# Kernel tuning notes

Hardware: AMD Instinct MI355X
Metric: run time of the kernel (lower is better)

The kernel has to match this reference:

```python
import jax, jax.numpy as jnp
import numpy as np

N = 100000
E = 3200000
K = 10
ALPHA = 0.1
EPS = 1e-5


def setup_inputs() -> dict:
    key = jax.random.key(0)
    ks = jax.random.split(key, 12)
    x = jax.random.normal(ks[0], (N, 512), dtype=jnp.float32)
    edge_index = jax.random.randint(ks[1], (2, E), 0, N, dtype=jnp.int32)
    w1 = jax.random.normal(ks[2], (128, 512), dtype=jnp.float32) * 0.02
    b1 = jnp.zeros((128,), jnp.float32)
    g1 = jnp.ones((128,), jnp.float32)
    be1 = jnp.zeros((128,), jnp.float32)
    m1 = jax.random.normal(ks[3], (128,), dtype=jnp.float32) * 0.1
    v1 = jax.random.uniform(ks[4], (128,), dtype=jnp.float32, minval=0.5, maxval=1.5)
    w2 = jax.random.normal(ks[5], (128, 128), dtype=jnp.float32) * 0.02
    b2 = jnp.zeros((128,), jnp.float32)
    g2 = jnp.ones((128,), jnp.float32)
    be2 = jnp.zeros((128,), jnp.float32)
    m2 = jax.random.normal(ks[6], (128,), dtype=jnp.float32) * 0.1
    v2 = jax.random.uniform(ks[7], (128,), dtype=jnp.float32, minval=0.5, maxval=1.5)
    w3 = jax.random.normal(ks[8], (3, 128), dtype=jnp.float32) * 0.02
    b3 = jnp.zeros((3,), jnp.float32)
    return dict(x=x, edge_index=edge_index, w1=w1, b1=b1, g1=g1, be1=be1, m1=m1, v1=v1,
                w2=w2, b2=b2, g2=g2, be2=be2, m2=m2, v2=v2, w3=w3, b3=b3)


def _bn(y, g, be, m, v):
    return (y - m) * jax.lax.rsqrt(v + EPS) * g + be


def reference(x, edge_index, w1, b1, g1, be1, m1, v1, w2, b2, g2, be2, m2, v2, w3, b3):
    # MLP (eval mode: BN uses running stats, dropout is identity)
    h = jax.nn.relu(_bn(x @ w1.T + b1, g1, be1, m1, v1))
    h = h + jax.nn.relu(_bn(h @ w2.T + b2, g2, be2, m2, v2))
    h = h @ w3.T + b3  # [N, 3]

    # APPNP propagation with GCN normalization + self-loops
    loop = jnp.arange(N, dtype=edge_index.dtype)
    src = jnp.concatenate([edge_index[0], loop])
    dst = jnp.concatenate([edge_index[1], loop])
    deg = jax.ops.segment_sum(jnp.ones_like(src, dtype=h.dtype), dst, num_segments=N)
    dinv = jnp.where(deg > 0, jax.lax.rsqrt(deg), 0.0)
    norm = dinv[src] * dinv[dst]  # [E+N]

    h0 = h
    z = h
    for _ in range(K):
        msg = z[src] * norm[:, None]
        z = jax.ops.segment_sum(msg, dst, num_segments=N)
        z = (1.0 - ALPHA) * z + ALPHA * h0
    return jax.nn.log_softmax(z, axis=1)
```

## Files before the change

### kernel.cpp

```cpp
#include <hip/hip_runtime.h>
#include <cstdint>
#include <cstddef>

#define N_NODES 100000
#define D_IN 512
#define ALPHA 0.1f
#define EPS_BN 1e-5f
#define M_TILE 128
#define BK 64

#define CBITS 8
#define CNODES 256
#define NCBIN 391
#define TILE 8192
#define EPT 32
#define BINCAP 9216

#define NPB 64
#define NB2 1563
#define LCAP3 3072

typedef float f32x4 __attribute__((ext_vector_type(4)));
typedef __bf16 bf16x8 __attribute__((ext_vector_type(8)));
typedef unsigned short u16x8 __attribute__((ext_vector_type(8)));
typedef unsigned short u16x4 __attribute__((ext_vector_type(4)));

__device__ __forceinline__ unsigned short f2bf(float f) {
  unsigned u = __float_as_uint(f);
  u += 0x7fffu + ((u >> 16) & 1u);
  return (unsigned short)(u >> 16);
}
__device__ __forceinline__ float bf2f(unsigned short h) {
  return __uint_as_float(((unsigned)h) << 16);
}

__global__ void k_prep(const float* __restrict__ w1, const float* __restrict__ b1,
                       const float* __restrict__ g1, const float* __restrict__ be1,
                       const float* __restrict__ m1, const float* __restrict__ v1,
                       const float* __restrict__ w2, const float* __restrict__ b2,
                       const float* __restrict__ g2, const float* __restrict__ be2,
                       const float* __restrict__ m2, const float* __restrict__ v2,
                       unsigned short* __restrict__ w1b, unsigned short* __restrict__ w2b,
                       float* __restrict__ bias1, float* __restrict__ bias2,
                       int* __restrict__ bincur) {
  int idx = blockIdx.x * 256 + threadIdx.x;
  if (idx < 65536) {
    int n = idx >> 9;
    float s = g1[n] * rsqrtf(v1[n] + EPS_BN);
    w1b[idx] = f2bf(w1[idx] * s);
  } else if (idx < 81920) {
    int i = idx - 65536;
    int n = i >> 7;
    float s = g2[n] * rsqrtf(v2[n] + EPS_BN);
    w2b[i] = f2bf(w2[i] * s);
  } else if (idx < 82048) {
    int c = idx - 81920;
    float s = g1[c] * rsqrtf(v1[c] + EPS_BN);
    bias1[c] = (b1[c] - m1[c]) * s + be1[c];
  } else if (idx < 82176) {
    int c = idx - 82048;
    float s = g2[c] * rsqrtf(v2[c] + EPS_BN);
    bias2[c] = (b2[c] - m2[c]) * s + be2[c];
  }
  int bi = idx - 82176;
  if (bi >= 0 && bi < NCBIN) bincur[bi] = 0;
}

#define NB_SCAN 391
__global__ void k_scan2(const int* __restrict__ bincur, int* __restrict__ bsum) {
  __shared__ int s[448];
  int t = threadIdx.x;
  for (int i = t; i < 448; i += 256) s[i] = (i < NB_SCAN) ? bincur[i] : 0;
  __syncthreads();
  if (t < 64) {
    int base = t * 7;
    int vals[7];
    int sum = 0;
#pragma unroll
    for (int j = 0; j < 7; ++j) { vals[j] = s[base + j]; sum += vals[j]; }
    int x = sum;
#pragma unroll
    for (int off = 1; off < 64; off <<= 1) {
      int y = __shfl_up(x, off, 64);
      if (t >= off) x += y;
    }
    int run = x - sum;
#pragma unroll
    for (int j = 0; j < 7; ++j) { int tmp = vals[j]; s[base + j] = run; run += tmp; }
  }
  __syncthreads();
  for (int i = t; i < NB_SCAN; i += 256) bsum[i] = s[i];
}

__global__ void k_scan3(const int* __restrict__ deg, const int* __restrict__ bsum,
                        int* __restrict__ row_start, float* __restrict__ dinv, int E) {
  __shared__ int sb[2][256];
  int t = threadIdx.x;
  int i = blockIdx.x * 256 + t;
  int d = (i < N_NODES) ? deg[i] : 0;
  sb[0][t] = d;
  __syncthreads();
  int cur = 0;
#pragma unroll
  for (int off = 1; off < 256; off <<= 1) {
    int val = sb[cur][t] + ((t >= off) ? sb[cur][t - off] : 0);
    sb[cur ^ 1][t] = val;
    __syncthreads();
    cur ^= 1;
  }
  int incl = sb[cur][t];
  int ex = incl - d;
  if (i < N_NODES) {
    int rs = bsum[blockIdx.x] + ex;
    row_start[i] = rs;
    dinv[i] = rsqrtf((float)(d + 1));
  }
  if (i == N_NODES) row_start[N_NODES] = E;
}

__global__ __launch_bounds__(256) void k_binA(const int* __restrict__ src,
                                              const int* __restrict__ dst, int E,
                                              int* __restrict__ bincur,
                                              unsigned* __restrict__ binned) {
  __shared__ unsigned stage[TILE];
  __shared__ int cnt[NCBIN];
  __shared__ int loff[NCBIN + 1];
  __shared__ int goff[NCBIN];
  __shared__ int sc[2][256];
  const int tid = threadIdx.x;

  for (int i = tid; i < NCBIN; i += 256) cnt[i] = 0;
  __syncthreads();

  const int e0 = blockIdx.x * TILE;
  const int n = min(TILE, E - e0);

  unsigned pk[EPT];
  int bp[EPT];
#pragma unroll
  for (int i = 0; i < EPT; ++i) {
    int o = i * 256 + tid;
    if (o < n) {
      int e = e0 + o;
      int d = dst[e];
      int s = src[e];
      int b = d >> CBITS;
      pk[i] = (unsigned)s | ((unsigned)(d & (CNODES - 1)) << 17);
      int p = atomicAdd(&cnt[b], 1);
      bp[i] = b | (p << 9);
    } else bp[i] = -1;
  }
  __syncthreads();

  int c0 = (2 * tid     < NCBIN) ? cnt[2 * tid]     : 0;
  int c1 = (2 * tid + 1 < NCBIN) ? cnt[2 * tid + 1] : 0;
  sc[0][tid] = c0 + c1;
  __syncthreads();
  int cur = 0;
#pragma unroll
  for (int off = 1; off < 256; off <<= 1) {
    sc[cur ^ 1][tid] = sc[cur][tid] + ((tid >= off) ? sc[cur][tid - off] : 0);
    __syncthreads();
    cur ^= 1;
  }
  int ex = sc[cur][tid] - (c0 + c1);
  if (2 * tid < NCBIN) loff[2 * tid] = ex;
  if (2 * tid + 1 < NCBIN) loff[2 * tid + 1] = ex + c0;
  if (tid == 255) loff[NCBIN] = sc[cur][255];
  __syncthreads();
  for (int i = tid; i < NCBIN; i += 256)
    if (cnt[i] > 0) goff[i] = atomicAdd(&bincur[i], cnt[i]);
  __syncthreads();

#pragma unroll
  for (int i = 0; i < EPT; ++i) {
    if (bp[i] >= 0) {
      int b = bp[i] & 511;
      int p = bp[i] >> 9;
      stage[loff[b] + p] = pk[i];
    }
  }
  __syncthreads();

  for (int i = tid; i < n; i += 256) {
    int lo = 0, hi = NCBIN;
    while (hi - lo > 1) { int mid = (lo + hi) >> 1; if (loff[mid] <= i) lo = mid; else hi = mid; }
    int b = lo;
    binned[(size_t)b * BINCAP + goff[b] + (i - loff[b])] = stage[i];
  }
}

__global__ __launch_bounds__(256) void k_binB1(const unsigned* __restrict__ binned,
                                               const int* __restrict__ bincur,
                                               int* __restrict__ deg) {
  __shared__ int lcnt[CNODES];
  int b = blockIdx.x;
  int t = threadIdx.x;
  lcnt[t] = 0;
  __syncthreads();
  int cnt = bincur[b];
  const unsigned* bp = binned + (size_t)b * BINCAP;
  for (int i = t; i < cnt; i += 256) {
    unsigned v = bp[i];
    atomicAdd(&lcnt[v >> 17], 1);
  }
  __syncthreads();
  int node = (b << CBITS) + t;
  if (node < N_NODES) deg[node] = lcnt[t];
}

__global__ __launch_bounds__(256) void k_binB2(const unsigned* __restrict__ binned,
                                               const int* __restrict__ bincur,
                                               const int* __restrict__ row_start,
                                               unsigned* __restrict__ csr_col) {
  __shared__ unsigned sortbuf[BINCAP];
  __shared__ int lcur[CNODES];
  int b = blockIdx.x;
  int t = threadIdx.x;
  int node0 = b << CBITS;
  int nodes = min(CNODES, N_NODES - node0);
  int rs0 = row_start[node0];
  if (t < nodes) lcur[t] = row_start[node0 + t] - rs0;
  __syncthreads();
  int cnt = bincur[b];
  const unsigned* bp = binned + (size_t)b * BINCAP;
  for (int i = t; i < cnt; i += 256) {
    unsigned v = bp[i];
    int p = atomicAdd(&lcur[v >> 17], 1);
    sortbuf[p] = v & 0x1FFFFu;
  }
  __syncthreads();
  for (int i = t; i < cnt; i += 256) csr_col[rs0 + i] = sortbuf[i];
}

__global__ __launch_bounds__(256, 2) void k_mlp(
    const float* __restrict__ x, const unsigned short* __restrict__ w1b,
    const unsigned short* __restrict__ w2b, const float* __restrict__ bias1,
    const float* __restrict__ bias2, const float* __restrict__ w3,
    const float* __restrict__ b3, const float* __restrict__ dinv,
    float4* __restrict__ h0, float4* __restrict__ zt) {
  __shared__ unsigned short arena[35840];
  __shared__ float lds_w3[384];
  unsigned short* lds_x = arena;
  unsigned short* lds_w = arena + 9216;
  unsigned short* lds_h = arena;
  unsigned short* lds_w2 = arena + 18432;

  const int tid = threadIdx.x;
  const int lane = tid & 63;
  const int wv = tid >> 6;
  const int fr = lane & 15;
  const int kq = (lane >> 4) * 8;
  const int rq = (lane >> 4) * 4;
  const int row0 = blockIdx.x * M_TILE;

  for (int i = tid; i < 384; i += 256) lds_w3[i] = w3[i];

#pragma unroll
  for (int it = 0; it < 8; ++it) {
    int idx = it * 256 + tid;
    int n = idx >> 4, c8 = idx & 15;
    uint4 v = *(const uint4*)(w2b + n * 128 + c8 * 8);
    *(uint4*)(lds_w2 + n * 136 + c8 * 8) = v;
  }

  const int xr_r = 0, xr_c = 0; (void)xr_r; (void)xr_c;
  f32x4 xr[8];
#pragma unroll
  for (int it = 0; it < 8; ++it) {
    int idx = it * 256 + tid;
    int r = idx >> 4, c4 = idx & 15;
    int gm = row0 + r;
    if (gm >= N_NODES) gm = N_NODES - 1;
    xr[it] = *(const f32x4*)(x + (size_t)gm * D_IN + 0 + c4 * 4);
  }

  f32x4 zero4 = {0.f, 0.f, 0.f, 0.f};
  f32x4 acc[2][8];
#pragma unroll
  for (int mt = 0; mt < 2; ++mt)
#pragma unroll
    for (int nt = 0; nt < 8; ++nt) acc[mt][nt] = zero4;

  for (int kb = 0; kb < D_IN; kb += BK) {
#pragma unroll
    for (int it = 0; it < 8; ++it) {
      int idx = it * 256 + tid;
      int r = idx >> 4, c4 = idx & 15;
      u16x4 o;
      o.x = f2bf(xr[it].x); o.y = f2bf(xr[it].y); o.z = f2bf(xr[it].z); o.w = f2bf(xr[it].w);
      *(u16x4*)(lds_x + r * 72 + c4 * 4) = o;
    }
#pragma unroll
    for (int it = 0; it < 4; ++it) {
      int idx = it * 256 + tid;
      int n = idx >> 3, c8 = idx & 7;
      uint4 v = *(const uint4*)(w1b + n * 512 + kb + c8 * 8);
      *(uint4*)(lds_w + n * 72 + c8 * 8) = v;
    }
    __syncthreads();
    if (kb + BK < D_IN) {
#pragma unroll
      for (int it = 0; it < 8; ++it) {
        int idx = it * 256 + tid;
        int r = idx >> 4, c4 = idx & 15;
        int gm = row0 + r;
        if (gm >= N_NODES) gm = N_NODES - 1;
        xr[it] = *(const f32x4*)(x + (size_t)gm * D_IN + (kb + BK) + c4 * 4);
      }
    }
#pragma unroll
    for (int kk = 0; kk < BK; kk += 32) {
      bf16x8 a[2], b[8];
#pragma unroll
      for (int mt = 0; mt < 2; ++mt)
        a[mt] = __builtin_bit_cast(bf16x8, *(const u16x8*)(lds_x + (wv * 32 + mt * 16 + fr) * 72 + kk + kq));
#pragma unroll
      for (int nt = 0; nt < 8; ++nt)
        b[nt] = __builtin_bit_cast(bf16x8, *(const u16x8*)(lds_w + (nt * 16 + fr) * 72 + kk + kq));
#pragma unroll
      for (int mt = 0; mt < 2; ++mt)
#pragma unroll
        for (int nt = 0; nt < 8; ++nt)
          acc[mt][nt] = __builtin_amdgcn_mfma_f32_16x16x32_bf16(a[mt], b[nt], acc[mt][nt], 0, 0, 0);
    }
    __syncthreads();
  }

  float b1v[8], b2v[8];
#pragma unroll
  for (int nt = 0; nt < 8; ++nt) {
    b1v[nt] = bias1[nt * 16 + fr];
    b2v[nt] = bias2[nt * 16 + fr];
  }
  float hr[2][8][4];
#pragma unroll
  for (int mt = 0; mt < 2; ++mt)
#pragma unroll
    for (int nt = 0; nt < 8; ++nt)
#pragma unroll
      for (int r = 0; r < 4; ++r) {
        int rl = wv * 32 + mt * 16 + rq + r;
        int cl = nt * 16 + fr;
        float h = acc[mt][nt][r] + b1v[nt];
        h = h > 0.f ? h : 0.f;
        hr[mt][nt][r] = h;
        lds_h[rl * 136 + cl] = f2bf(h);
      }
  __syncthreads();

  f32x4 acc2[2][8];
#pragma unroll
  for (int mt = 0; mt < 2; ++mt)
#pragma unroll
    for (int nt = 0; nt < 8; ++nt) acc2[mt][nt] = zero4;
#pragma unroll
  for (int kk = 0; kk < 128; kk += 32) {
    bf16x8 a[2], b[8];
#pragma unroll
    for (int mt = 0; mt < 2; ++mt)
      a[mt] = __builtin_bit_cast(bf16x8, *(const u16x8*)(lds_h + (wv * 32 + mt * 16 + fr) * 136 + kk + kq));
#pragma unroll
    for (int nt = 0; nt < 8; ++nt)
      b[nt] = __builtin_bit_cast(bf16x8, *(const u16x8*)(lds_w2 + (nt * 16 + fr) * 136 + kk + kq));
#pragma unroll
    for (int mt = 0; mt < 2; ++mt)
#pragma unroll
      for (int nt = 0; nt < 8; ++nt)
        acc2[mt][nt] = __builtin_amdgcn_mfma_f32_16x16x32_bf16(a[mt], b[nt], acc2[mt][nt], 0, 0, 0);
  }
  __syncthreads();

#pragma unroll
  for (int mt = 0; mt < 2; ++mt)
#pragma unroll
    for (int nt = 0; nt < 8; ++nt)
#pragma unroll
      for (int r = 0; r < 4; ++r) {
        int rl = wv * 32 + mt * 16 + rq + r;
        int cl = nt * 16 + fr;
        float t2 = acc2[mt][nt][r] + b2v[nt];
        t2 = t2 > 0.f ? t2 : 0.f;
        lds_h[rl * 136 + cl] = f2bf(hr[mt][nt][r] + t2);
      }
  __syncthreads();

  if (tid < 128) {
    int m = tid;
    int gm = row0 + m;
    if (gm < N_NODES) {
      float a0 = 0.f, a1 = 0.f, a2 = 0.f;
#pragma unroll 8
      for (int c = 0; c < 128; ++c) {
        float hv = bf2f(lds_h[m * 136 + c]);
        a0 += hv * lds_w3[c];
        a1 += hv * lds_w3[128 + c];
        a2 += hv * lds_w3[256 + c];
      }
      float z0 = a0 + b3[0], z1 = a1 + b3[1], z2 = a2 + b3[2];
      float di = dinv[gm];
      h0[gm] = make_float4(z0, z1, z2, 0.f);
      zt[gm] = make_float4(di * z0, di * z1, di * z2, 0.f);
    }
  }
}

#define GATHER_BODY(IDX)                                                        \
  for (; j + 8 <= je; j += 8) {                                                 \
    unsigned c0 = IDX(j + 0), c1 = IDX(j + 1), c2 = IDX(j + 2), c3 = IDX(j + 3);\
    unsigned c4 = IDX(j + 4), c5 = IDX(j + 5), c6 = IDX(j + 6), c7 = IDX(j + 7);\
    float4 v0 = zin[c0], v1 = zin[c1], v2 = zin[c2], v3 = zin[c3];              \
    float4 v4 = zin[c4], v5 = zin[c5], v6 = zin[c6], v7 = zin[c7];              \
    sx += ((v0.x + v1.x) + (v2.x + v3.x)) + ((v4.x + v5.x) + (v6.x + v7.x));    \
    sy += ((v0.y + v1.y) + (v2.y + v3.y)) + ((v4.y + v5.y) + (v6.y + v7.y));    \
    sz += ((v0.z + v1.z) + (v2.z + v3.z)) + ((v4.z + v5.z) + (v6.z + v7.z));    \
  }                                                                             \
  if (j + 4 <= je) {                                                            \
    unsigned c0 = IDX(j + 0), c1 = IDX(j + 1), c2 = IDX(j + 2), c3 = IDX(j + 3);\
    float4 v0 = zin[c0], v1 = zin[c1], v2 = zin[c2], v3 = zin[c3];              \
    sx += (v0.x + v1.x) + (v2.x + v3.x);                                        \
    sy += (v0.y + v1.y) + (v2.y + v3.y);                                        \
    sz += (v0.z + v1.z) + (v2.z + v3.z);                                        \
    j += 4;                                                                     \
  }                                                                             \
  if (j + 2 <= je) {                                                            \
    unsigned c0 = IDX(j + 0), c1 = IDX(j + 1);                                  \
    float4 v0 = zin[c0], v1 = zin[c1];                                          \
    sx += v0.x + v1.x; sy += v0.y + v1.y; sz += v0.z + v1.z;                    \
    j += 2;                                                                     \
  }                                                                             \
  if (j < je) {                                                                 \
    float4 v = zin[IDX(j)];                                                     \
    sx += v.x; sy += v.y; sz += v.z;                                            \
  }

template <bool FINAL>
__global__ __launch_bounds__(256) void k_iter2(
    const float4* __restrict__ zin, float4* __restrict__ zout,
    const int* __restrict__ row_start, const unsigned* __restrict__ csr_col,
    const float* __restrict__ dinv, const float4* __restrict__ h0v,
    float* __restrict__ out) {
  __shared__ unsigned lidx[LCAP3];
  __shared__ float psum[3][NPB][3];
  __shared__ int srs[2];
  const int t = threadIdx.x;
  const int q = t >> 6;
  const int tn = t & 63;
  const int node0 = blockIdx.x * NPB;
  const int node = node0 + tn;
  const bool valid = node < N_NODES;

  if (t == 0) srs[0] = row_start[node0];
  if (t == 1) srs[1] = row_start[min(node0 + NPB, N_NODES)];
  __syncthreads();
  const int rs0 = srs[0];
  const int cnt = srs[1] - rs0;
  const bool use_lds = (cnt <= LCAP3);
  if (use_lds) {
    for (int i = t; i < cnt; i += 256) lidx[i] = csr_col[rs0 + i];
  }

  int jb = 0, je = 0;
  if (valid) {
    int r0 = row_start[node];
    int r1 = row_start[node + 1];
    int len = r1 - r0;
    jb = r0 + ((len * q) >> 2);
    je = r0 + ((len * (q + 1)) >> 2);
  }
  __syncthreads();

  float sx = 0.f, sy = 0.f, sz = 0.f;
  if (use_lds) {
    int j = jb - rs0;
    je -= rs0;
#define IDXL(J) lidx[J]
    GATHER_BODY(IDXL)
#undef IDXL
  } else {
    int j = jb;
#define IDXG(J) csr_col[J]
    GATHER_BODY(IDXG)
#undef IDXG
  }

  if (q) { psum[q - 1][tn][0] = sx; psum[q - 1][tn][1] = sy; psum[q - 1][tn][2] = sz; }
  __syncthreads();
  if (q == 0 && valid) {
    float4 self = zin[node];
    float4 h = h0v[node];
    float di = dinv[node];
    sx += (psum[0][tn][0] + psum[1][tn][0]) + (psum[2][tn][0] + self.x);
    sy += (psum[0][tn][1] + psum[1][tn][1]) + (psum[2][tn][1] + self.y);
    sz += (psum[0][tn][2] + psum[1][tn][2]) + (psum[2][tn][2] + self.z);
    float zx = (1.f - ALPHA) * di * sx + ALPHA * h.x;
    float zy = (1.f - ALPHA) * di * sy + ALPHA * h.y;
    float zz = (1.f - ALPHA) * di * sz + ALPHA * h.z;
    if (!FINAL) {
      zout[node] = make_float4(di * zx, di * zy, di * zz, 0.f);
    } else {
      float mx = fmaxf(zx, fmaxf(zy, zz));
      float l = logf(expf(zx - mx) + expf(zy - mx) + expf(zz - mx));
      out[node * 3 + 0] = zx - mx - l;
      out[node * 3 + 1] = zy - mx - l;
      out[node * 3 + 2] = zz - mx - l;
    }
  }
}

extern "C" void kernel_launch(void* const* d_in, const int* in_sizes, int n_in,
                              void* d_out, int out_size, void* d_ws, size_t ws_size,
                              hipStream_t stream) {
  const float* x   = (const float*)d_in[0];
  const int*   ei  = (const int*)d_in[1];
  const float* w1  = (const float*)d_in[2];
  const float* b1  = (const float*)d_in[3];
  const float* g1  = (const float*)d_in[4];
  const float* be1 = (const float*)d_in[5];
  const float* m1  = (const float*)d_in[6];
  const float* v1  = (const float*)d_in[7];
  const float* w2  = (const float*)d_in[8];
  const float* b2  = (const float*)d_in[9];
  const float* g2  = (const float*)d_in[10];
  const float* be2 = (const float*)d_in[11];
  const float* m2  = (const float*)d_in[12];
  const float* v2  = (const float*)d_in[13];
  const float* w3  = (const float*)d_in[14];
  const float* b3  = (const float*)d_in[15];

  const int E = in_sizes[1] / 2;
  const int* srcA = ei;
  const int* dstA = ei + E;

  char* w = (char*)d_ws;
  size_t off = 0;
  auto alloc = [&](size_t bytes) -> void* {
    void* p = w + off;
    off = (off + bytes + 255) & ~(size_t)255;
    return p;
  };
  unsigned short* w1b   = (unsigned short*)alloc(65536 * 2);
  unsigned short* w2b   = (unsigned short*)alloc(16384 * 2);
  float* bias1          = (float*)alloc(128 * 4);
  float* bias2          = (float*)alloc(128 * 4);
  int*   deg            = (int*)alloc((size_t)N_NODES * 4);
  int*   row_start      = (int*)alloc(((size_t)N_NODES + 1) * 4);
  float* dinv           = (float*)alloc((size_t)N_NODES * 4);
  int*   bsum           = (int*)alloc(512 * 4);
  int*   bincur         = (int*)alloc((size_t)NCBIN * 4);
  float4* h0            = (float4*)alloc((size_t)N_NODES * 16);
  float4* ztA           = (float4*)alloc((size_t)N_NODES * 16);
  float4* ztB           = (float4*)alloc((size_t)N_NODES * 16);
  unsigned* csr_col     = (unsigned*)alloc((size_t)E * 4);
  unsigned* binned      = (unsigned*)alloc((size_t)NCBIN * BINCAP * 4);

  const int NB = (N_NODES + 255) / 256;
  const int NTILE = (E + TILE - 1) / TILE;

  k_prep<<<(82176 + NCBIN + 255) / 256, 256, 0, stream>>>(
      w1, b1, g1, be1, m1, v1, w2, b2, g2, be2, m2, v2, w1b, w2b, bias1, bias2, bincur);
  k_binA<<<NTILE, 256, 0, stream>>>(srcA, dstA, E, bincur, binned);
  k_binB1<<<NCBIN, 256, 0, stream>>>(binned, bincur, deg);
  k_scan2<<<1, 256, 0, stream>>>(bincur, bsum);
  k_scan3<<<NB, 256, 0, stream>>>(deg, bsum, row_start, dinv, E);
  k_binB2<<<NCBIN, 256, 0, stream>>>(binned, bincur, row_start, csr_col);
  k_mlp<<<(N_NODES + M_TILE - 1) / M_TILE, 256, 0, stream>>>(
      x, w1b, w2b, bias1, bias2, w3, b3, dinv, h0, ztA);

  const float4* zin = ztA;
  float4* zout = ztB;
  for (int k = 0; k < 9; ++k) {
    k_iter2<false><<<NB2, 256, 0, stream>>>(zin, zout, row_start, csr_col, dinv, h0, nullptr);
    const float4* tswap = zout;
    zout = (float4*)zin;
    zin = tswap;
  }
  k_iter2<true><<<NB2, 256, 0, stream>>>(zin, nullptr, row_start, csr_col, dinv, h0, (float*)d_out);
}
```

Before: 596.5 us.

## Balance APPNP gather by splitting each block's edge range evenly across threads

Replaces the per-node, four-way split gather with an edge-balanced scheme. Each thread takes a contiguous slice of the block's edges staged in LDS, issues up to 12 independent loads up front, and binary-searches the row offsets to find its starting node. Partial sums are then flushed into per-node LDS accumulators with shared-memory atomics. This aims to remove load imbalance between nodes and raise memory-level parallelism, at the cost of redundant clamped loads, LDS atomic contention and a summation order that is no longer fixed.

```diff
diff --git a/kernel.cpp b/kernel.cpp
--- a/kernel.cpp
+++ b/kernel.cpp
@@ -19,6 +19,7 @@
 #define NPB 64
 #define NB2 1563
 #define LCAP3 3072
+#define PMAX 12
 
 typedef float f32x4 __attribute__((ext_vector_type(4)));
 typedef __bf16 bf16x8 __attribute__((ext_vector_type(8)));
@@ -264,7 +265,6 @@
     *(uint4*)(lds_w2 + n * 136 + c8 * 8) = v;
   }
 
-  const int xr_r = 0, xr_c = 0; (void)xr_r; (void)xr_c;
   f32x4 xr[8];
 #pragma unroll
   for (int it = 0; it < 8; ++it) {
@@ -405,94 +405,87 @@
   }
 }
 
-#define GATHER_BODY(IDX)                                                        \
-  for (; j + 8 <= je; j += 8) {                                                 \
-    unsigned c0 = IDX(j + 0), c1 = IDX(j + 1), c2 = IDX(j + 2), c3 = IDX(j + 3);\
-    unsigned c4 = IDX(j + 4), c5 = IDX(j + 5), c6 = IDX(j + 6), c7 = IDX(j + 7);\
-    float4 v0 = zin[c0], v1 = zin[c1], v2 = zin[c2], v3 = zin[c3];              \
-    float4 v4 = zin[c4], v5 = zin[c5], v6 = zin[c6], v7 = zin[c7];              \
-    sx += ((v0.x + v1.x) + (v2.x + v3.x)) + ((v4.x + v5.x) + (v6.x + v7.x));    \
-    sy += ((v0.y + v1.y) + (v2.y + v3.y)) + ((v4.y + v5.y) + (v6.y + v7.y));    \
-    sz += ((v0.z + v1.z) + (v2.z + v3.z)) + ((v4.z + v5.z) + (v6.z + v7.z));    \
-  }                                                                             \
-  if (j + 4 <= je) {                                                            \
-    unsigned c0 = IDX(j + 0), c1 = IDX(j + 1), c2 = IDX(j + 2), c3 = IDX(j + 3);\
-    float4 v0 = zin[c0], v1 = zin[c1], v2 = zin[c2], v3 = zin[c3];              \
-    sx += (v0.x + v1.x) + (v2.x + v3.x);                                        \
-    sy += (v0.y + v1.y) + (v2.y + v3.y);                                        \
-    sz += (v0.z + v1.z) + (v2.z + v3.z);                                        \
-    j += 4;                                                                     \
-  }                                                                             \
-  if (j + 2 <= je) {                                                            \
-    unsigned c0 = IDX(j + 0), c1 = IDX(j + 1);                                  \
-    float4 v0 = zin[c0], v1 = zin[c1];                                          \
-    sx += v0.x + v1.x; sy += v0.y + v1.y; sz += v0.z + v1.z;                    \
-    j += 2;                                                                     \
-  }                                                                             \
-  if (j < je) {                                                                 \
-    float4 v = zin[IDX(j)];                                                     \
-    sx += v.x; sy += v.y; sz += v.z;                                            \
-  }
-
 template <bool FINAL>
-__global__ __launch_bounds__(256) void k_iter2(
+__global__ __launch_bounds__(256) void k_iter3(
     const float4* __restrict__ zin, float4* __restrict__ zout,
     const int* __restrict__ row_start, const unsigned* __restrict__ csr_col,
     const float* __restrict__ dinv, const float4* __restrict__ h0v,
     float* __restrict__ out) {
   __shared__ unsigned lidx[LCAP3];
-  __shared__ float psum[3][NPB][3];
-  __shared__ int srs[2];
+  __shared__ int row_off[NPB + 1];
+  __shared__ float accs[NPB][3];
   const int t = threadIdx.x;
-  const int q = t >> 6;
-  const int tn = t & 63;
   const int node0 = blockIdx.x * NPB;
-  const int node = node0 + tn;
-  const bool valid = node < N_NODES;
-
-  if (t == 0) srs[0] = row_start[node0];
-  if (t == 1) srs[1] = row_start[min(node0 + NPB, N_NODES)];
-  __syncthreads();
-  const int rs0 = srs[0];
-  const int cnt = srs[1] - rs0;
-  const bool use_lds = (cnt <= LCAP3);
-  if (use_lds) {
+  const int node = node0 + t;
+
+  if (t <= NPB) row_off[t] = row_start[min(node0 + t, N_NODES)];
+  if (t < NPB) { accs[t][0] = 0.f; accs[t][1] = 0.f; accs[t][2] = 0.f; }
+  __syncthreads();
+  const int rs0 = row_off[0];
+  const int cnt = row_off[NPB] - rs0;
+
+  if (cnt <= LCAP3) {
     for (int i = t; i < cnt; i += 256) lidx[i] = csr_col[rs0 + i];
-  }
-
-  int jb = 0, je = 0;
-  if (valid) {
-    int r0 = row_start[node];
-    int r1 = row_start[node + 1];
-    int len = r1 - r0;
-    jb = r0 + ((len * q) >> 2);
-    je = r0 + ((len * (q + 1)) >> 2);
-  }
-  __syncthreads();
-
-  float sx = 0.f, sy = 0.f, sz = 0.f;
-  if (use_lds) {
-    int j = jb - rs0;
-    je -= rs0;
-#define IDXL(J) lidx[J]
-    GATHER_BODY(IDXL)
-#undef IDXL
+    __syncthreads();
+
+    const int per = (cnt + 255) >> 8;
+    const int e0 = t * per;
+    const int e1 = min(e0 + per, cnt);
+    if (e0 < e1) {
+      f32x4 v[PMAX];
+#pragma unroll
+      for (int i = 0; i < PMAX; ++i) {
+        int e = e0 + i;
+        unsigned c = lidx[(e < e1) ? e : (e1 - 1)];
+        v[i] = *(const f32x4*)(zin + c);
+      }
+      int lo = 0, hi = NPB;
+      while (hi - lo > 1) {
+        int m = (lo + hi) >> 1;
+        if (row_off[m] - rs0 <= e0) lo = m; else hi = m;
+      }
+      int r = lo;
+      int nb = row_off[r + 1] - rs0;
+      float sx = 0.f, sy = 0.f, sz = 0.f;
+#pragma unroll
+      for (int i = 0; i < PMAX; ++i) {
+        int e = e0 + i;
+        if (e < e1) {
+          while (e >= nb) {
+            atomicAdd(&accs[r][0], sx);
+            atomicAdd(&accs[r][1], sy);
+            atomicAdd(&accs[r][2], sz);
+            sx = 0.f; sy = 0.f; sz = 0.f;
+            ++r;
+            nb = row_off[r + 1] - rs0;
+          }
+          sx += v[i].x; sy += v[i].y; sz += v[i].z;
+        }
+      }
+      atomicAdd(&accs[r][0], sx);
+      atomicAdd(&accs[r][1], sy);
+      atomicAdd(&accs[r][2], sz);
+    }
   } else {
-    int j = jb;
-#define IDXG(J) csr_col[J]
-    GATHER_BODY(IDXG)
-#undef IDXG
-  }
-
-  if (q) { psum[q - 1][tn][0] = sx; psum[q - 1][tn][1] = sy; psum[q - 1][tn][2] = sz; }
-  __syncthreads();
-  if (q == 0 && valid) {
+    if (t < NPB && node < N_NODES) {
+      int r0 = row_start[node], r1 = row_start[node + 1];
+      float sx = 0.f, sy = 0.f, sz = 0.f;
+      for (int j = r0; j < r1; ++j) {
+        float4 vv = zin[csr_col[j]];
+        sx += vv.x; sy += vv.y; sz += vv.z;
+      }
+      accs[t][0] = sx; accs[t][1] = sy; accs[t][2] = sz;
+    }
+  }
+  __syncthreads();
+
+  if (t < NPB && node < N_NODES) {
     float4 self = zin[node];
     float4 h = h0v[node];
     float di = dinv[node];
-    sx += (psum[0][tn][0] + psum[1][tn][0]) + (psum[2][tn][0] + self.x);
-    sy += (psum[0][tn][1] + psum[1][tn][1]) + (psum[2][tn][1] + self.y);
-    sz += (psum[0][tn][2] + psum[1][tn][2]) + (psum[2][tn][2] + self.z);
+    float sx = accs[t][0] + self.x;
+    float sy = accs[t][1] + self.y;
+    float sz = accs[t][2] + self.z;
     float zx = (1.f - ALPHA) * di * sx + ALPHA * h.x;
     float zy = (1.f - ALPHA) * di * sy + ALPHA * h.y;
     float zz = (1.f - ALPHA) * di * sz + ALPHA * h.z;
@@ -570,10 +563,10 @@
   const float4* zin = ztA;
   float4* zout = ztB;
   for (int k = 0; k < 9; ++k) {
-    k_iter2<false><<<NB2, 256, 0, stream>>>(zin, zout, row_start, csr_col, dinv, h0, nullptr);
+    k_iter3<false><<<NB2, 256, 0, stream>>>(zin, zout, row_start, csr_col, dinv, h0, nullptr);
     const float4* tswap = zout;
     zout = (float4*)zin;
     zin = tswap;
   }
-  k_iter2<true><<<NB2, 256, 0, stream>>>(zin, nullptr, row_start, csr_col, dinv, h0, (float*)d_out);
-}
+  k_iter3<true><<<NB2, 256, 0, stream>>>(zin, nullptr, row_start, csr_col, dinv, h0, (float*)d_out);
+}
```

After: 668.0 us. 1.12x slower.

## Store propagated features as packed fp16 and fuse CSR build kernels

Applied to the files above, without the earlier changes.

The propagation state z is now stored as three fp16 values packed into 8 bytes instead of a float4. This halves the bytes moved by each random gather in the ten propagation iterations. Separately, the degree count, the two scan kernels and the CSR scatter are merged into one per-bin kernel, which computes its prefix offset by summing earlier bin counts directly. Using fp16 adds rounding error to the iterated values, and each block now does a redundant partial sum over bincur.

```diff
diff --git a/kernel.cpp b/kernel.cpp
--- a/kernel.cpp
+++ b/kernel.cpp
@@ -24,6 +24,7 @@
 typedef __bf16 bf16x8 __attribute__((ext_vector_type(8)));
 typedef unsigned short u16x8 __attribute__((ext_vector_type(8)));
 typedef unsigned short u16x4 __attribute__((ext_vector_type(4)));
+typedef unsigned long long u64;
 
 __device__ __forceinline__ unsigned short f2bf(float f) {
   unsigned u = __float_as_uint(f);
@@ -32,6 +33,19 @@
 }
 __device__ __forceinline__ float bf2f(unsigned short h) {
   return __uint_as_float(((unsigned)h) << 16);
+}
+
+__device__ __forceinline__ u64 pk3(float x, float y, float z) {
+  unsigned short a = __builtin_bit_cast(unsigned short, (_Float16)x);
+  unsigned short b = __builtin_bit_cast(unsigned short, (_Float16)y);
+  unsigned short c = __builtin_bit_cast(unsigned short, (_Float16)z);
+  return (u64)a | ((u64)b << 16) | ((u64)c << 32);
+}
+__device__ __forceinline__ void up3(u64 p, float& sx, float& sy, float& sz) {
+  unsigned lo = (unsigned)p, hi = (unsigned)(p >> 32);
+  sx += (float)__builtin_bit_cast(_Float16, (unsigned short)(lo & 0xFFFFu));
+  sy += (float)__builtin_bit_cast(_Float16, (unsigned short)(lo >> 16));
+  sz += (float)__builtin_bit_cast(_Float16, (unsigned short)(hi & 0xFFFFu));
 }
 
 __global__ void k_prep(const float* __restrict__ w1, const float* __restrict__ b1,
@@ -66,58 +80,6 @@
   if (bi >= 0 && bi < NCBIN) bincur[bi] = 0;
 }
 
-#define NB_SCAN 391
-__global__ void k_scan2(const int* __restrict__ bincur, int* __restrict__ bsum) {
-  __shared__ int s[448];
-  int t = threadIdx.x;
-  for (int i = t; i < 448; i += 256) s[i] = (i < NB_SCAN) ? bincur[i] : 0;
-  __syncthreads();
-  if (t < 64) {
-    int base = t * 7;
-    int vals[7];
-    int sum = 0;
-#pragma unroll
-    for (int j = 0; j < 7; ++j) { vals[j] = s[base + j]; sum += vals[j]; }
-    int x = sum;
-#pragma unroll
-    for (int off = 1; off < 64; off <<= 1) {
-      int y = __shfl_up(x, off, 64);
-      if (t >= off) x += y;
-    }
-    int run = x - sum;
-#pragma unroll
-    for (int j = 0; j < 7; ++j) { int tmp = vals[j]; s[base + j] = run; run += tmp; }
-  }
-  __syncthreads();
-  for (int i = t; i < NB_SCAN; i += 256) bsum[i] = s[i];
-}
-
-__global__ void k_scan3(const int* __restrict__ deg, const int* __restrict__ bsum,
-                        int* __restrict__ row_start, float* __restrict__ dinv, int E) {
-  __shared__ int sb[2][256];
-  int t = threadIdx.x;
-  int i = blockIdx.x * 256 + t;
-  int d = (i < N_NODES) ? deg[i] : 0;
-  sb[0][t] = d;
-  __syncthreads();
-  int cur = 0;
-#pragma unroll
-  for (int off = 1; off < 256; off <<= 1) {
-    int val = sb[cur][t] + ((t >= off) ? sb[cur][t - off] : 0);
-    sb[cur ^ 1][t] = val;
-    __syncthreads();
-    cur ^= 1;
-  }
-  int incl = sb[cur][t];
-  int ex = incl - d;
-  if (i < N_NODES) {
-    int rs = bsum[blockIdx.x] + ex;
-    row_start[i] = rs;
-    dinv[i] = rsqrtf((float)(d + 1));
-  }
-  if (i == N_NODES) row_start[N_NODES] = E;
-}
-
 __global__ __launch_bounds__(256) void k_binA(const int* __restrict__ src,
                                               const int* __restrict__ dst, int E,
                                               int* __restrict__ bincur,
@@ -190,42 +152,63 @@
   }
 }
 
-__global__ __launch_bounds__(256) void k_binB1(const unsigned* __restrict__ binned,
-                                               const int* __restrict__ bincur,
-                                               int* __restrict__ deg) {
+__global__ __launch_bounds__(256) void k_binB(const unsigned* __restrict__ binned,
+                                              const int* __restrict__ bincur,
+                                              int* __restrict__ row_start,
+                                              float* __restrict__ dinv,
+                                              unsigned* __restrict__ csr_col, int E) {
+  __shared__ unsigned ebuf[BINCAP];
+  __shared__ unsigned sortbuf[BINCAP];
   __shared__ int lcnt[CNODES];
-  int b = blockIdx.x;
-  int t = threadIdx.x;
+  __shared__ int lcur[CNODES];
+  __shared__ int sb[2][256];
+  __shared__ int red[4];
+  const int b = blockIdx.x;
+  const int t = threadIdx.x;
+
+  int part = 0;
+  for (int i = t; i < b; i += 256) part += bincur[i];
+#pragma unroll
+  for (int off = 32; off > 0; off >>= 1) part += __shfl_down(part, off, 64);
+  if ((t & 63) == 0) red[t >> 6] = part;
   lcnt[t] = 0;
   __syncthreads();
+  const int rs0 = (red[0] + red[1]) + (red[2] + red[3]);
   int cnt = bincur[b];
+  if (cnt > BINCAP) cnt = BINCAP;
+
   const unsigned* bp = binned + (size_t)b * BINCAP;
   for (int i = t; i < cnt; i += 256) {
     unsigned v = bp[i];
+    ebuf[i] = v;
     atomicAdd(&lcnt[v >> 17], 1);
   }
   __syncthreads();
-  int node = (b << CBITS) + t;
-  if (node < N_NODES) deg[node] = lcnt[t];
-}
-
-__global__ __launch_bounds__(256) void k_binB2(const unsigned* __restrict__ binned,
-                                               const int* __restrict__ bincur,
-                                               const int* __restrict__ row_start,
-                                               unsigned* __restrict__ csr_col) {
-  __shared__ unsigned sortbuf[BINCAP];
-  __shared__ int lcur[CNODES];
-  int b = blockIdx.x;
-  int t = threadIdx.x;
-  int node0 = b << CBITS;
-  int nodes = min(CNODES, N_NODES - node0);
-  int rs0 = row_start[node0];
-  if (t < nodes) lcur[t] = row_start[node0 + t] - rs0;
-  __syncthreads();
-  int cnt = bincur[b];
-  const unsigned* bp = binned + (size_t)b * BINCAP;
+
+  sb[0][t] = lcnt[t];
+  __syncthreads();
+  int cur = 0;
+#pragma unroll
+  for (int off = 1; off < 256; off <<= 1) {
+    sb[cur ^ 1][t] = sb[cur][t] + ((t >= off) ? sb[cur][t - off] : 0);
+    __syncthreads();
+    cur ^= 1;
+  }
+  int ex = sb[cur][t] - lcnt[t];
+
+  const int node0 = b << CBITS;
+  const int node = node0 + t;
+  if (node < N_NODES) {
+    row_start[node] = rs0 + ex;
+    dinv[node] = rsqrtf((float)(lcnt[t] + 1));
+  }
+  if (node == N_NODES) row_start[N_NODES] = E;
+  if (b == NCBIN - 1 && t == 255) row_start[N_NODES] = E;
+  lcur[t] = ex;
+  __syncthreads();
+
   for (int i = t; i < cnt; i += 256) {
-    unsigned v = bp[i];
+    unsigned v = ebuf[i];
     int p = atomicAdd(&lcur[v >> 17], 1);
     sortbuf[p] = v & 0x1FFFFu;
   }
@@ -238,7 +221,7 @@
     const unsigned short* __restrict__ w2b, const float* __restrict__ bias1,
     const float* __restrict__ bias2, const float* __restrict__ w3,
     const float* __restrict__ b3, const float* __restrict__ dinv,
-    float4* __restrict__ h0, float4* __restrict__ zt) {
+    float4* __restrict__ h0, u64* __restrict__ zt) {
   __shared__ unsigned short arena[35840];
   __shared__ float lds_w3[384];
   unsigned short* lds_x = arena;
@@ -264,7 +247,6 @@
     *(uint4*)(lds_w2 + n * 136 + c8 * 8) = v;
   }
 
-  const int xr_r = 0, xr_c = 0; (void)xr_r; (void)xr_c;
   f32x4 xr[8];
 #pragma unroll
   for (int it = 0; it < 8; ++it) {
@@ -400,43 +382,39 @@
       float z0 = a0 + b3[0], z1 = a1 + b3[1], z2 = a2 + b3[2];
       float di = dinv[gm];
       h0[gm] = make_float4(z0, z1, z2, 0.f);
-      zt[gm] = make_float4(di * z0, di * z1, di * z2, 0.f);
+      zt[gm] = pk3(di * z0, di * z1, di * z2);
     }
   }
 }
 
 #define GATHER_BODY(IDX)                                                        \
   for (; j + 8 <= je; j += 8) {                                                 \
-    unsigned c0 = IDX(j + 0), c1 = IDX(j + 1), c2 = IDX(j + 2), c3 = IDX(j + 3);\
-    unsigned c4 = IDX(j + 4), c5 = IDX(j + 5), c6 = IDX(j + 6), c7 = IDX(j + 7);\
-    float4 v0 = zin[c0], v1 = zin[c1], v2 = zin[c2], v3 = zin[c3];              \
-    float4 v4 = zin[c4], v5 = zin[c5], v6 = zin[c6], v7 = zin[c7];              \
-    sx += ((v0.x + v1.x) + (v2.x + v3.x)) + ((v4.x + v5.x) + (v6.x + v7.x));    \
-    sy += ((v0.y + v1.y) + (v2.y + v3.y)) + ((v4.y + v5.y) + (v6.y + v7.y));    \
-    sz += ((v0.z + v1.z) + (v2.z + v3.z)) + ((v4.z + v5.z) + (v6.z + v7.z));    \
+    u64 p0 = zin[IDX(j + 0)], p1 = zin[IDX(j + 1)];                             \
+    u64 p2 = zin[IDX(j + 2)], p3 = zin[IDX(j + 3)];                             \
+    u64 p4 = zin[IDX(j + 4)], p5 = zin[IDX(j + 5)];                             \
+    u64 p6 = zin[IDX(j + 6)], p7 = zin[IDX(j + 7)];                             \
+    up3(p0, sx, sy, sz); up3(p1, sx, sy, sz);                                   \
+    up3(p2, sx, sy, sz); up3(p3, sx, sy, sz);                                   \
+    up3(p4, sx, sy, sz); up3(p5, sx, sy, sz);                                   \
+    up3(p6, sx, sy, sz); up3(p7, sx, sy, sz);                                   \
   }                                                                             \
   if (j + 4 <= je) {                                                            \
-    unsigned c0 = IDX(j + 0), c1 = IDX(j + 1), c2 = IDX(j + 2), c3 = IDX(j + 3);\
-    float4 v0 = zin[c0], v1 = zin[c1], v2 = zin[c2], v3 = zin[c3];              \
-    sx += (v0.x + v1.x) + (v2.x + v3.x);                                        \
-    sy += (v0.y + v1.y) + (v2.y + v3.y);                                        \
-    sz += (v0.z + v1.z) + (v2.z + v3.z);                                        \
+    u64 p0 = zin[IDX(j + 0)], p1 = zin[IDX(j + 1)];                             \
+    u64 p2 = zin[IDX(j + 2)], p3 = zin[IDX(j + 3)];                             \
+    up3(p0, sx, sy, sz); up3(p1, sx, sy, sz);                                   \
+    up3(p2, sx, sy, sz); up3(p3, sx, sy, sz);                                   \
     j += 4;                                                                     \
   }                                                                             \
   if (j + 2 <= je) {                                                            \
-    unsigned c0 = IDX(j + 0), c1 = IDX(j + 1);                                  \
-    float4 v0 = zin[c0], v1 = zin[c1];                                          \
-    sx += v0.x + v1.x; sy += v0.y + v1.y; sz += v0.z + v1.z;                    \
+    u64 p0 = zin[IDX(j + 0)], p1 = zin[IDX(j + 1)];                             \
+    up3(p0, sx, sy, sz); up3(p1, sx, sy, sz);                                   \
     j += 2;                                                                     \
   }                                                                             \
-  if (j < je) {                                                                 \
-    float4 v = zin[IDX(j)];                                                     \
-    sx += v.x; sy += v.y; sz += v.z;                                            \
-  }
+  if (j < je) { u64 p0 = zin[IDX(j)]; up3(p0, sx, sy, sz); }
 
 template <bool FINAL>
 __global__ __launch_bounds__(256) void k_iter2(
-    const float4* __restrict__ zin, float4* __restrict__ zout,
+    const u64* __restrict__ zin, u64* __restrict__ zout,
     const int* __restrict__ row_start, const unsigned* __restrict__ csr_col,
     const float* __restrict__ dinv, const float4* __restrict__ h0v,
     float* __restrict__ out) {
@@ -487,17 +465,17 @@
   if (q) { psum[q - 1][tn][0] = sx; psum[q - 1][tn][1] = sy; psum[q - 1][tn][2] = sz; }
   __syncthreads();
   if (q == 0 && valid) {
-    float4 self = zin[node];
+    up3(zin[node], sx, sy, sz);
     float4 h = h0v[node];
     float di = dinv[node];
-    sx += (psum[0][tn][0] + psum[1][tn][0]) + (psum[2][tn][0] + self.x);
-    sy += (psum[0][tn][1] + psum[1][tn][1]) + (psum[2][tn][1] + self.y);
-    sz += (psum[0][tn][2] + psum[1][tn][2]) + (psum[2][tn][2] + self.z);
+    sx += (psum[0][tn][0] + psum[1][tn][0]) + psum[2][tn][0];
+    sy += (psum[0][tn][1] + psum[1][tn][1]) + psum[2][tn][1];
+    sz += (psum[0][tn][2] + psum[1][tn][2]) + psum[2][tn][2];
     float zx = (1.f - ALPHA) * di * sx + ALPHA * h.x;
     float zy = (1.f - ALPHA) * di * sy + ALPHA * h.y;
     float zz = (1.f - ALPHA) * di * sz + ALPHA * h.z;
     if (!FINAL) {
-      zout[node] = make_float4(di * zx, di * zy, di * zz, 0.f);
+      zout[node] = pk3(di * zx, di * zy, di * zz);
     } else {
       float mx = fmaxf(zx, fmaxf(zy, zz));
       float l = logf(expf(zx - mx) + expf(zy - mx) + expf(zz - mx));
@@ -543,36 +521,30 @@
   unsigned short* w2b   = (unsigned short*)alloc(16384 * 2);
   float* bias1          = (float*)alloc(128 * 4);
   float* bias2          = (float*)alloc(128 * 4);
-  int*   deg            = (int*)alloc((size_t)N_NODES * 4);
   int*   row_start      = (int*)alloc(((size_t)N_NODES + 1) * 4);
   float* dinv           = (float*)alloc((size_t)N_NODES * 4);
-  int*   bsum           = (int*)alloc(512 * 4);
   int*   bincur         = (int*)alloc((size_t)NCBIN * 4);
   float4* h0            = (float4*)alloc((size_t)N_NODES * 16);
-  float4* ztA           = (float4*)alloc((size_t)N_NODES * 16);
-  float4* ztB           = (float4*)alloc((size_t)N_NODES * 16);
+  u64*   ztA            = (u64*)alloc((size_t)N_NODES * 8);
+  u64*   ztB            = (u64*)alloc((size_t)N_NODES * 8);
   unsigned* csr_col     = (unsigned*)alloc((size_t)E * 4);
   unsigned* binned      = (unsigned*)alloc((size_t)NCBIN * BINCAP * 4);
 
-  const int NB = (N_NODES + 255) / 256;
   const int NTILE = (E + TILE - 1) / TILE;
 
   k_prep<<<(82176 + NCBIN + 255) / 256, 256, 0, stream>>>(
       w1, b1, g1, be1, m1, v1, w2, b2, g2, be2, m2, v2, w1b, w2b, bias1, bias2, bincur);
   k_binA<<<NTILE, 256, 0, stream>>>(srcA, dstA, E, bincur, binned);
-  k_binB1<<<NCBIN, 256, 0, stream>>>(binned, bincur, deg);
-  k_scan2<<<1, 256, 0, stream>>>(bincur, bsum);
-  k_scan3<<<NB, 256, 0, stream>>>(deg, bsum, row_start, dinv, E);
-  k_binB2<<<NCBIN, 256, 0, stream>>>(binned, bincur, row_start, csr_col);
+  k_binB<<<NCBIN, 256, 0, stream>>>(binned, bincur, row_start, dinv, csr_col, E);
   k_mlp<<<(N_NODES + M_TILE - 1) / M_TILE, 256, 0, stream>>>(
       x, w1b, w2b, bias1, bias2, w3, b3, dinv, h0, ztA);
 
-  const float4* zin = ztA;
-  float4* zout = ztB;
+  const u64* zin = ztA;
+  u64* zout = ztB;
   for (int k = 0; k < 9; ++k) {
     k_iter2<false><<<NB2, 256, 0, stream>>>(zin, zout, row_start, csr_col, dinv, h0, nullptr);
-    const float4* tswap = zout;
-    zout = (float4*)zin;
+    const u64* tswap = zout;
+    zout = (u64*)zin;
     zin = tswap;
   }
   k_iter2<true><<<NB2, 256, 0, stream>>>(zin, nullptr, row_start, csr_col, dinv, h0, (float*)d_out);
```

Result: faster. 572.5 us (-4.0%).
